# Kernel tuning notes

Hardware: AMD Instinct MI355X
Metric: run time of the kernel (lower is better)

The kernel has to match this reference:

```python
import jax, jax.numpy as jnp
import numpy as np

NHEAD = 16
EPS = 1e-6

def _phi_norm(x):
    # phi = silu, then L2 normalize over last dim (torch F.normalize: x / max(||x||, eps))
    x = jax.nn.silu(x)
    n = jnp.linalg.norm(x, axis=-1, keepdims=True)
    return x / jnp.maximum(n, EPS)

def setup_inputs() -> dict:
    key = jax.random.key(0)
    k1, k2, k3 = jax.random.split(key, 3)
    B, M, N, D = 4, 1024, 2048, 1024
    q = jax.random.normal(k1, (B, M, D), dtype=jnp.float32)
    kv = jax.random.normal(k2, (B, N, D), dtype=jnp.float32)
    kv_mask = jax.random.bernoulli(k3, 0.1, (B, N))  # True = masked out
    return {"q": q, "kv": kv, "kv_mask": kv_mask}

def reference(q, kv, kv_mask):
    B, M, D = q.shape
    N = kv.shape[1]
    dh = D // NHEAD
    # [B, H, M, dh] / [B, H, N, dh]
    qh = q.reshape(B, M, NHEAD, dh).transpose(0, 2, 1, 3)
    kh = kv.reshape(B, N, NHEAD, dh).transpose(0, 2, 1, 3)
    vh = kh  # values are raw kv heads (no phi/norm)
    qh_n = _phi_norm(qh)
    kh_n = _phi_norm(kh)
    scores = jnp.einsum('bhmd,bhnd->bhmn', qh_n, kh_n) / jnp.sqrt(jnp.asarray(dh, qh_n.dtype))
    scores = jnp.where(kv_mask[:, None, None, :], -jnp.inf, scores)
    attn = jax.nn.softmax(scores.astype(jnp.float32), axis=-1).astype(scores.dtype)
    out = jnp.einsum('bhmn,bhnd->bhmd', attn, vh)
    return out.transpose(0, 2, 1, 3).reshape(B, M, D)
```

## Files before the change

### kernel.cpp

```cpp
#include <hip/hip_runtime.h>
#include <hip/hip_bf16.h>
#include <cmath>
#include <stdint.h>

#define B_ 4
#define M_ 1024
#define N_ 2048
#define D_ 1024
#define H_ 16
#define DH_ 64
#define NT 64
#define NTH 16
#define PITCH 72

typedef __bf16 bf16_t;
typedef __attribute__((ext_vector_type(8))) __bf16 bf16x8;
typedef __attribute__((ext_vector_type(16))) float f32x16;
typedef __attribute__((ext_vector_type(2))) float f32x2;

static __device__ __forceinline__ float silu_f(float x) {
  return x / (1.0f + __expf(-x));
}

static __device__ __forceinline__ unsigned pk2(float a, float b) {
  union { __bf16 h[2]; unsigned u; } p;
  p.h[0] = (__bf16)a; p.h[1] = (__bf16)b;
  return p.u;
}

static __device__ __forceinline__ int sw23(int x) {
  return (x & ~12) | ((x & 4) << 1) | ((x & 8) >> 1);
}

__global__ __launch_bounds__(256) void prep_kernel(
    const float* __restrict__ kv, const int* __restrict__ kv_mask,
    bf16_t* __restrict__ kp, bf16_t* __restrict__ vt,
    unsigned long long* __restrict__ mb) {
  __shared__ __align__(16) bf16_t Lt[NT][PITCH];
  const int bx = blockIdx.x;
  const int hp = bx & 7;
  const int nt = (bx >> 3) & 31;
  const int b  = bx >> 8;
  const int n0 = nt * NT;
  const int tid = threadIdx.x;
  const float keep = kv_mask[b * N_ + n0 + (tid >> 2)] ? 0.f : 1.f;

  #pragma unroll
  for (int hi = 0; hi < 2; ++hi) {
    const int h = hp * 2 + hi;
    const size_t bh = (size_t)(b * H_ + h);
    {
      const int r = tid >> 2, c0 = (tid & 3) * 16;
      const float* src = kv + ((size_t)(b * N_ + n0 + r)) * D_ + h * DH_ + c0;
      union { float f[16]; float4 v4[4]; } raw;
      raw.v4[0] = *(const float4*)(src + 0);
      raw.v4[1] = *(const float4*)(src + 4);
      raw.v4[2] = *(const float4*)(src + 8);
      raw.v4[3] = *(const float4*)(src + 12);
      float sv[16];
      float ss = 0.f;
      #pragma unroll
      for (int i = 0; i < 16; ++i) { sv[i] = silu_f(raw.f[i]); ss += sv[i] * sv[i]; }
      ss += __shfl_xor(ss, 1); ss += __shfl_xor(ss, 2);
      const float inv = keep / fmaxf(sqrtf(ss), 1e-6f);
      union { bf16_t bs[16]; uint4 u[2]; } pk;
      #pragma unroll
      for (int i = 0; i < 16; ++i) pk.bs[i] = (bf16_t)(sv[i] * inv);
      const size_t fbase = bh * 131072 +
          (size_t)((nt * 8 + (r >> 5) * 4 + (tid & 3)) * 512 + sw23(r & 31) * 8);
      *(uint4*)(kp + fbase)       = pk.u[0];
      *(uint4*)(kp + fbase + 256) = pk.u[1];
      union { bf16_t bs[16]; uint4 u[2]; } pv;
      #pragma unroll
      for (int i = 0; i < 16; ++i) pv.bs[i] = (bf16_t)(raw.f[i] * keep);
      uint4* ldst = (uint4*)&Lt[r][c0];
      ldst[0] = pv.u[0]; ldst[1] = pv.u[1];
    }
    __syncthreads();
    {
      const int f = tid >> 5;
      const int i_ = f >> 2, ks = f & 3;
      const int vl = tid & 31;
      const int d = i_ * 32 + vl;
      const size_t vbase = bh * 131072 + (size_t)((nt * 8 + f) * 512);
      #pragma unroll
      for (int hi2 = 0; hi2 < 2; ++hi2) {
        union { bf16_t bs[8]; uint4 u; } vp;
        #pragma unroll
        for (int j = 0; j < 8; ++j) vp.bs[j] = Lt[ks * 16 + hi2 * 8 + j][d];
        *(uint4*)(vt + vbase + (hi2 * 32 + vl) * 8) = vp.u;
      }
    }
    __syncthreads();
  }
  if (bx == 0 && tid < B_ * (N_ / 64)) {
    const int b2 = tid >> 5, tt = tid & 31;
    unsigned long long m = 0ull;
    for (int i = 0; i < 64; ++i)
      if (kv_mask[b2 * N_ + tt * 64 + i]) m |= (1ull << i);
    mb[tid] = m;
  }
}

__global__ __launch_bounds__(512, 4) void attn_kernel(
    const float* __restrict__ q, const bf16_t* __restrict__ kp,
    const bf16_t* __restrict__ vt, const unsigned long long* __restrict__ mb,
    float* __restrict__ out) {
  __shared__ __align__(1024) char smem[33280];

  const int tid  = threadIdx.x;
  const int w    = tid >> 6;
  const int wq   = w & 3;
  const int half = w >> 2;
  const int lane = tid & 63;
  const int l31  = lane & 31;
  const int hi   = lane >> 5;

  const int wg = (blockIdx.x & 7) * 64 + (blockIdx.x >> 3);
  const int bh = wg >> 3;
  const int m0 = (wg & 7) * 128;
  const int b = bh >> 4, h = bh & 15;

  const bf16_t* kfb = kp + (size_t)bh * 131072 + (size_t)half * 65536
                         + (size_t)lane * 8;
  const bf16_t* vfb = vt + (size_t)bh * 131072 + (size_t)half * 65536
                         + (size_t)lane * 8;

  bf16x8 ka[2][4];
  #pragma unroll
  for (int nb = 0; nb < 2; ++nb)
    #pragma unroll
    for (int kk = 0; kk < 4; ++kk)
      ka[nb][kk] = *(const bf16x8*)(kfb + (nb * 4 + kk) * 512);

  bf16x8 qb[4];
  {
    const float* qrow =
        q + ((size_t)(b * M_ + m0 + wq * 32 + l31)) * D_ + h * DH_ + hi * 8;
    float sv[32];
    float ss = 0.f;
    #pragma unroll
    for (int kk = 0; kk < 4; ++kk) {
      float4 a0 = *(const float4*)(qrow + kk * 16);
      float4 a1 = *(const float4*)(qrow + kk * 16 + 4);
      sv[kk * 8 + 0] = silu_f(a0.x); sv[kk * 8 + 1] = silu_f(a0.y);
      sv[kk * 8 + 2] = silu_f(a0.z); sv[kk * 8 + 3] = silu_f(a0.w);
      sv[kk * 8 + 4] = silu_f(a1.x); sv[kk * 8 + 5] = silu_f(a1.y);
      sv[kk * 8 + 6] = silu_f(a1.z); sv[kk * 8 + 7] = silu_f(a1.w);
      #pragma unroll
      for (int i = 0; i < 8; ++i) ss += sv[kk * 8 + i] * sv[kk * 8 + i];
    }
    ss += __shfl_xor(ss, 32);
    const float inv = 0.125f / fmaxf(sqrtf(ss), 1e-6f);
    #pragma unroll
    for (int kk = 0; kk < 4; ++kk) {
      union { unsigned u[4]; bf16x8 v; } pq;
      #pragma unroll
      for (int jj = 0; jj < 4; ++jj)
        pq.u[jj] = pk2(sv[kk * 8 + jj * 2] * inv, sv[kk * 8 + jj * 2 + 1] * inv);
      qb[kk] = pq.v;
    }
  }

  f32x16 o0, o1;
  #pragma unroll
  for (int r = 0; r < 16; ++r) { o0[r] = 0.f; o1[r] = 0.f; }
  float lrun = 0.f;
  unsigned cl = 0, ch = 0;
  const unsigned long long* mbb = mb + b * (N_ / 64);

  #pragma unroll 1
  for (int tt = 0; tt < NTH; ++tt) {
    const unsigned long long mk = mbb[half * NTH + tt];
    cl += (unsigned)__popcll(mk & 0x00FF00FF00FF00FFULL);
    ch += (unsigned)__popcll(mk & 0xFF00FF00FF00FF00ULL);

    bf16x8 pa[4];
    #pragma unroll
    for (int nb = 0; nb < 2; ++nb) {
      f32x16 s;
      #pragma unroll
      for (int r = 0; r < 16; ++r) s[r] = 0.f;
      __builtin_amdgcn_s_setprio(1);
      #pragma unroll
      for (int kk = 0; kk < 4; ++kk)
        s = __builtin_amdgcn_mfma_f32_32x32x16_bf16(ka[nb][kk], qb[kk], s, 0, 0, 0);
      __builtin_amdgcn_s_setprio(0);

      f32x2 p2[8];
      #pragma unroll
      for (int i = 0; i < 8; ++i) {
        f32x2 x; x.x = s[2 * i]; x.y = s[2 * i + 1];
        f32x2 u = x * 0.5f + 1.0f;
        p2[i] = x * u + 1.0f;
      }
      f32x2 t0 = (p2[0] + p2[1]) + (p2[2] + p2[3]);
      f32x2 t1 = (p2[4] + p2[5]) + (p2[6] + p2[7]);
      f32x2 ts = t0 + t1;
      lrun += ts.x + ts.y;

      union { unsigned u[4]; bf16x8 v; } f0, f1;
      #pragma unroll
      for (int jj = 0; jj < 4; ++jj) {
        f0.u[jj] = pk2(p2[jj].x, p2[jj].y);
        f1.u[jj] = pk2(p2[4 + jj].x, p2[4 + jj].y);
      }
      pa[nb * 2]     = f0.v;
      pa[nb * 2 + 1] = f1.v;
    }

    const bf16_t* vfp = vfb + (size_t)tt * 4096;
    bf16x8 va[4];
    #pragma unroll
    for (int ks = 0; ks < 4; ++ks)
      va[ks] = *(const bf16x8*)(vfp + ks * 512);
    {
      const bf16_t* kn = kfb + (size_t)((tt + 1) & 15) * 4096;
      #pragma unroll
      for (int nb = 0; nb < 2; ++nb)
        #pragma unroll
        for (int kk = 0; kk < 4; ++kk)
          ka[nb][kk] = *(const bf16x8*)(kn + (nb * 4 + kk) * 512);
    }

    __builtin_amdgcn_s_setprio(1);
    #pragma unroll
    for (int ks = 0; ks < 4; ++ks)
      o0 = __builtin_amdgcn_mfma_f32_32x32x16_bf16(va[ks], pa[ks], o0, 0, 0, 0);
    __builtin_amdgcn_s_setprio(0);

    #pragma unroll
    for (int ks = 0; ks < 4; ++ks)
      va[ks] = *(const bf16x8*)(vfp + (4 + ks) * 512);
    __builtin_amdgcn_s_setprio(1);
    #pragma unroll
    for (int ks = 0; ks < 4; ++ks)
      o1 = __builtin_amdgcn_mfma_f32_32x32x16_bf16(va[ks], pa[ks], o1, 0, 0, 0);
    __builtin_amdgcn_s_setprio(0);
  }

  lrun -= (float)(hi ? ch : cl);
  lrun += __shfl_xor(lrun, 32);

  __syncthreads();
  float* Ob = (float*)smem;
  float* Lb = (float*)(smem + 32768);

  if (half == 0) {
    #pragma unroll
    for (int r = 0; r < 16; ++r) {
      const int d = (r & 3) + ((r >> 2) << 3) + (hi << 2);
      Ob[d * 128 + wq * 32 + l31]        = o0[r];
      Ob[(d + 32) * 128 + wq * 32 + l31] = o1[r];
    }
    if (hi == 0) Lb[wq * 32 + l31] = lrun;
  }
  __syncthreads();
  if (half == 1) {
    #pragma unroll
    for (int r = 0; r < 16; ++r) {
      const int d = (r & 3) + ((r >> 2) << 3) + (hi << 2);
      Ob[d * 128 + wq * 32 + l31]        += o0[r];
      Ob[(d + 32) * 128 + wq * 32 + l31] += o1[r];
    }
    if (hi == 0) Lb[wq * 32 + l31] += lrun;
  }
  __syncthreads();
  {
    const int m = tid >> 2, dc = (tid & 3) * 16;
    const float lv = Lb[m];
    const float iv = lv > 0.f ? 1.0f / lv : 0.f;
    float* orow = out + ((size_t)(b * M_ + m0 + m)) * D_ + h * DH_ + dc;
    #pragma unroll
    for (int i0 = 0; i0 < 16; i0 += 4) {
      float4 v;
      v.x = Ob[(dc + i0 + 0) * 128 + m] * iv;
      v.y = Ob[(dc + i0 + 1) * 128 + m] * iv;
      v.z = Ob[(dc + i0 + 2) * 128 + m] * iv;
      v.w = Ob[(dc + i0 + 3) * 128 + m] * iv;
      *(float4*)(orow + i0) = v;
    }
  }
}

extern "C" void kernel_launch(void* const* d_in, const int* in_sizes, int n_in,
                              void* d_out, int out_size, void* d_ws, size_t ws_size,
                              hipStream_t stream) {
  const float* q  = (const float*)d_in[0];
  const float* kv = (const float*)d_in[1];
  const int* kv_mask = (const int*)d_in[2];
  float* out = (float*)d_out;

  bf16_t* kp = (bf16_t*)d_ws;
  bf16_t* vt = kp + (size_t)B_ * H_ * N_ * DH_;
  unsigned long long* mb =
      (unsigned long long*)((char*)d_ws + 2 * (size_t)B_ * H_ * N_ * DH_ * sizeof(bf16_t));

  prep_kernel<<<B_ * 32 * 8, 256, 0, stream>>>(kv, kv_mask, kp, vt, mb);
  attn_kernel<<<B_ * H_ * (M_ / 128), 512, 0, stream>>>(q, kp, vt, mb, out);
}
```

Measured before the change: 146.1 us.

## Stagger per-wave K/V tile order, prefetch V earlier, interleave PV MFMAs

Each wave in the group now starts its sweep over the 16 KV tiles at a different offset (wq*4), so waves of the same block read different tiles at any moment instead of all hitting the same addresses. Both halves of the V tile are loaded at the top of each iteration, ahead of the QK MFMAs, to give the loads more time to land. The two PV accumulator chains are interleaved so independent MFMAs alternate. The QK accumulator now starts from a zero vector fed into the first MFMA. The cost is more live VGPRs for the eight V fragments, which could lower occupancy, and less shared cache reuse across waves because they no longer touch the same tile together.

```diff
diff --git a/kernel.cpp b/kernel.cpp
--- a/kernel.cpp
+++ b/kernel.cpp
@@ -126,12 +126,14 @@
   const bf16_t* vfb = vt + (size_t)bh * 131072 + (size_t)half * 65536
                          + (size_t)lane * 8;
 
+  const int tst = wq * 4;
+
   bf16x8 ka[2][4];
   #pragma unroll
   for (int nb = 0; nb < 2; ++nb)
     #pragma unroll
     for (int kk = 0; kk < 4; ++kk)
-      ka[nb][kk] = *(const bf16x8*)(kfb + (nb * 4 + kk) * 512);
+      ka[nb][kk] = *(const bf16x8*)(kfb + (size_t)tst * 4096 + (nb * 4 + kk) * 512);
 
   bf16x8 qb[4];
   {
@@ -162,28 +164,36 @@
     }
   }
 
-  f32x16 o0, o1;
+  f32x16 o0, o1, zvec;
   #pragma unroll
-  for (int r = 0; r < 16; ++r) { o0[r] = 0.f; o1[r] = 0.f; }
+  for (int r = 0; r < 16; ++r) { o0[r] = 0.f; o1[r] = 0.f; zvec[r] = 0.f; }
   float lrun = 0.f;
   unsigned cl = 0, ch = 0;
   const unsigned long long* mbb = mb + b * (N_ / 64);
 
   #pragma unroll 1
-  for (int tt = 0; tt < NTH; ++tt) {
+  for (int t = 0; t < NTH; ++t) {
+    const int tt = (t + tst) & 15;
     const unsigned long long mk = mbb[half * NTH + tt];
     cl += (unsigned)__popcll(mk & 0x00FF00FF00FF00FFULL);
     ch += (unsigned)__popcll(mk & 0xFF00FF00FF00FF00ULL);
 
+    const bf16_t* vfp = vfb + (size_t)tt * 4096;
+    bf16x8 va0[4], va1[4];
+    #pragma unroll
+    for (int ks = 0; ks < 4; ++ks) {
+      va0[ks] = *(const bf16x8*)(vfp + ks * 512);
+      va1[ks] = *(const bf16x8*)(vfp + (4 + ks) * 512);
+    }
+
     bf16x8 pa[4];
     #pragma unroll
     for (int nb = 0; nb < 2; ++nb) {
-      f32x16 s;
-      #pragma unroll
-      for (int r = 0; r < 16; ++r) s[r] = 0.f;
       __builtin_amdgcn_s_setprio(1);
-      #pragma unroll
-      for (int kk = 0; kk < 4; ++kk)
+      f32x16 s = __builtin_amdgcn_mfma_f32_32x32x16_bf16(
+          ka[nb][0], qb[0], zvec, 0, 0, 0);
+      #pragma unroll
+      for (int kk = 1; kk < 4; ++kk)
         s = __builtin_amdgcn_mfma_f32_32x32x16_bf16(ka[nb][kk], qb[kk], s, 0, 0, 0);
       __builtin_amdgcn_s_setprio(0);
 
@@ -209,11 +219,6 @@
       pa[nb * 2 + 1] = f1.v;
     }
 
-    const bf16_t* vfp = vfb + (size_t)tt * 4096;
-    bf16x8 va[4];
-    #pragma unroll
-    for (int ks = 0; ks < 4; ++ks)
-      va[ks] = *(const bf16x8*)(vfp + ks * 512);
     {
       const bf16_t* kn = kfb + (size_t)((tt + 1) & 15) * 4096;
       #pragma unroll
@@ -225,17 +230,10 @@
 
     __builtin_amdgcn_s_setprio(1);
     #pragma unroll
-    for (int ks = 0; ks < 4; ++ks)
-      o0 = __builtin_amdgcn_mfma_f32_32x32x16_bf16(va[ks], pa[ks], o0, 0, 0, 0);
-    __builtin_amdgcn_s_setprio(0);
-
-    #pragma unroll
-    for (int ks = 0; ks < 4; ++ks)
-      va[ks] = *(const bf16x8*)(vfp + (4 + ks) * 512);
-    __builtin_amdgcn_s_setprio(1);
-    #pragma unroll
-    for (int ks = 0; ks < 4; ++ks)
-      o1 = __builtin_amdgcn_mfma_f32_32x32x16_bf16(va[ks], pa[ks], o1, 0, 0, 0);
+    for (int ks = 0; ks < 4; ++ks) {
+      o0 = __builtin_amdgcn_mfma_f32_32x32x16_bf16(va0[ks], pa[ks], o0, 0, 0, 0);
+      o1 = __builtin_amdgcn_mfma_f32_32x32x16_bf16(va1[ks], pa[ks], o1, 0, 0, 0);
+    }
     __builtin_amdgcn_s_setprio(0);
   }
 
```

Measured after the change: 205.0 us. 40.3% more time.
